# Optimization experiments

Hardware: AMD Instinct MI355X
Metric: run time of the kernel (lower is better)

The kernel has to match this reference:

```python
import jax, jax.numpy as jnp
import numpy as np

E = 256; H = 8; HD = E // H
L_LEN = 300; A_LEN = 250
T = 768; B = 4
NEG = -1e9


def setup_inputs() -> dict:
    rng = jax.random.key(0)
    ks = jax.random.split(rng, 16)
    n = lambda k, s, sc=1.0: jax.random.normal(k, s, dtype=jnp.float32) * sc
    return {
        "query": n(ks[0], (T, B, E)),
        "key": n(ks[1], (T, B, E)),
        "value": n(ks[2], (T, B, E)),
        "in_proj_w": n(ks[3], (3 * E, E), 0.05),
        "in_proj_b": jnp.zeros((3 * E,), jnp.float32),
        "out_w": n(ks[4], (7, E, E), 0.05),
        "out_b": jnp.zeros((7, E), jnp.float32),
        "s_l_w": n(ks[5], (E, 4 * E), 0.05),
        "s_l_b": jnp.zeros((E,), jnp.float32),
        "s_a_w": n(ks[6], (E, 4 * E), 0.05),
        "s_a_b": jnp.zeros((E,), jnp.float32),
        "s_v_w": n(ks[7], (E, 4 * E), 0.05),
        "s_v_b": jnp.zeros((E,), jnp.float32),
        "final_w": n(ks[8], (E, E), 0.05),
        "final_b": jnp.zeros((E,), jnp.float32),
    }


def _forward(query, key, value, in_proj_w, in_proj_b, out_w, out_b,
             s_l_w, s_l_b, s_a_w, s_a_b, s_v_w, s_v_b, final_w, final_b):
    t, b, e = query.shape
    scaling = HD ** -0.5
    Wq, Wk, Wv = in_proj_w[:E], in_proj_w[E:2 * E], in_proj_w[2 * E:]
    bq, bk, bv = in_proj_b[:E], in_proj_b[E:2 * E], in_proj_b[2 * E:]
    q = (query @ Wq.T + bq) * scaling
    k = key @ Wk.T + bk
    v = value @ Wv.T + bv
    # (T, B, E) -> (B*H, T, HD)
    sh = lambda x: x.reshape(t, b * H, HD).transpose(1, 0, 2)
    q, k, v = sh(q), sh(k), sh(v)
    # shared QK^T, reused by all 7 masked branches
    scores = jnp.einsum('bth,bsh->bts', q, k)  # (B*H, T, T)
    idx = jnp.arange(t)
    seg = jnp.where(idx < L_LEN, 0, jnp.where(idx < L_LEN + A_LEN, 1, 2))

    def branch(i, mods):
        # m[j] = 1 iff position j belongs to one of the selected modalities
        m = sum((seg == s) for s in mods).astype(scores.dtype)  # (T,)
        # additive mask: in-set query attends only in-set keys; out-of-set
        # query rows get all -1e9 (uniform softmax, zeroed by row mask below)
        add = jnp.where((m[:, None] * m[None, :]) > 0, 0.0, NEG)
        w = jax.nn.softmax(scores + add, axis=-1) * m[None, :, None]
        o = jnp.einsum('bts,bsh->bth', w, v * m[None, :, None])
        o = o.transpose(1, 0, 2).reshape(t, b, e)
        return o @ out_w[i].T + out_b[i]

    attn_lav = branch(0, (0, 1, 2))
    attn_la = branch(1, (0, 1))
    attn_lv = branch(2, (0, 2))
    attn_av = branch(3, (1, 2))
    attn_l = branch(4, (0,))
    attn_a = branch(5, (1,))
    attn_v = branch(6, (2,))

    sl = jnp.concatenate([attn_lav, attn_la, attn_lv, attn_l], -1) @ s_l_w.T + s_l_b
    sa = jnp.concatenate([attn_lav, attn_la, attn_av, attn_a], -1) @ s_a_w.T + s_a_b
    sv = jnp.concatenate([attn_lav, attn_lv, attn_av, attn_v], -1) @ s_v_w.T + s_v_b
    return (sl + sa + sv) @ final_w.T + final_b


def reference(query, key, value, in_proj_w, in_proj_b, out_w, out_b,
              s_l_w, s_l_b, s_a_w, s_a_b, s_v_w, s_v_b, final_w, final_b):
    return _forward(query, key, value, in_proj_w, in_proj_b, out_w, out_b,
                    s_l_w, s_l_b, s_a_w, s_a_b, s_v_w, s_v_b, final_w, final_b)
```

## Files before the change

### kernel.cpp

```cpp
#include <hip/hip_runtime.h>
#include <hip/hip_bf16.h>

#define E 256
#define H 8
#define HD 32
#define T 768
#define B 4
#define BH 32

typedef __attribute__((ext_vector_type(8))) short bf16x8;
typedef __attribute__((ext_vector_type(4))) float f32x4;
typedef __attribute__((ext_vector_type(16))) float f32x16;

__device__ __forceinline__ float b2f(__hip_bfloat16 x) { return __bfloat162float(x); }

__device__ __forceinline__ unsigned short f2bf_u(float x) {
    __hip_bfloat16 h = __float2bfloat16(x);
    return *(unsigned short*)&h;
}
__device__ __forceinline__ float bfu2f(unsigned short u) {
    return __uint_as_float(((unsigned int)u) << 16);
}

__device__ __forceinline__ int detect_f32(const void* query) {
    const unsigned short* q = (const unsigned short*)query;
    int lane = threadIdx.x & 63;
    int bad = 0;
    #pragma unroll
    for (int i = 0; i < 4; ++i) {
        float v = bfu2f(q[lane + i * 64]);
        bad |= (!(v == v) || fabsf(v) > 1e4f) ? 1 : 0;
    }
    return __any(bad) ? 1 : 0;
}

__device__ __forceinline__ void f8_split(const float* v, bf16x8& h, bf16x8& l) {
    #pragma unroll
    for (int e = 0; e < 8; ++e) {
        unsigned short hu = f2bf_u(v[e]);
        h[e] = (short)hu;
        l[e] = (short)f2bf_u(v[e] - bfu2f(hu));
    }
}

#define MFMA3(ACC, AH, AL, BH_, BL_)                                         \
    ACC = __builtin_amdgcn_mfma_f32_16x16x32_bf16(AH, BH_, ACC, 0, 0, 0);    \
    ACC = __builtin_amdgcn_mfma_f32_16x16x32_bf16(AH, BL_, ACC, 0, 0, 0);    \
    ACC = __builtin_amdgcn_mfma_f32_16x16x32_bf16(AL, BH_, ACC, 0, 0, 0);

#define MFMA3W(ACC, AH, AL, BH_, BL_)                                        \
    ACC = __builtin_amdgcn_mfma_f32_32x32x16_bf16(AH, BH_, ACC, 0, 0, 0);    \
    ACC = __builtin_amdgcn_mfma_f32_32x32x16_bf16(AH, BL_, ACC, 0, 0, 0);    \
    ACC = __builtin_amdgcn_mfma_f32_32x32x16_bf16(AL, BH_, ACC, 0, 0, 0);

__device__ __forceinline__ bf16x8 mk8(int a, int b, int c, int d) {
    union { int i[4]; bf16x8 v; } u;
    u.i[0] = a; u.i[1] = b; u.i[2] = c; u.i[3] = d;
    return u.v;
}

__device__ __forceinline__ float ldu(const void* p, size_t i, int f32) {
    if (f32) return ((const float*)p)[i];
    return b2f(((const __hip_bfloat16*)p)[i]);
}

__device__ __forceinline__ float gsum_load(int i, int r2, int r,
                                           const void* sl, const void* sa,
                                           const void* sv, int f32)
{
    size_t base = (size_t)r2 * 1024;
    switch (i) {
        case 0: return ldu(sl, base + r, f32) + ldu(sa, base + r, f32) + ldu(sv, base + r, f32);
        case 1: return ldu(sl, base + 256 + r, f32) + ldu(sa, base + 256 + r, f32);
        case 2: return ldu(sl, base + 512 + r, f32) + ldu(sv, base + 256 + r, f32);
        case 3: return ldu(sa, base + 512 + r, f32) + ldu(sv, base + 512 + r, f32);
        case 4: return ldu(sl, base + 768 + r, f32);
        case 5: return ldu(sa, base + 768 + r, f32);
        default: return ldu(sv, base + 768 + r, f32);
    }
}

__global__ __launch_bounds__(256) void stage1_kernel(
    const void* query, const void* w,
    const void* sl, const void* sa, const void* sv, const void* outw,
    const void* outb, const void* slb, const void* sab, const void* svb,
    unsigned short* __restrict__ WFh, unsigned short* __restrict__ WFl,
    unsigned short* __restrict__ GFh, unsigned short* __restrict__ GFl,
    unsigned short* __restrict__ OWFh, unsigned short* __restrict__ OWFl,
    float* __restrict__ c0)
{
    __shared__ float red[256];
    int f32 = detect_f32(query);
    if (blockIdx.x < 544) {
        int item = blockIdx.x * 256 + threadIdx.x;
        if (item < 24576) {
            int gc = item >> 5, kg = item & 31;
            float v[8];
            if (f32) {
                const float4* p = (const float4*)((const float*)w +
                                   (size_t)gc * 256 + kg * 8);
                *(float4*)&v[0] = p[0];
                *(float4*)&v[4] = p[1];
            } else {
                #pragma unroll
                for (int j = 0; j < 8; ++j)
                    v[j] = ldu(w, (size_t)gc * 256 + kg * 8 + j, 0);
            }
            bf16x8 h, l;
            f8_split(v, h, l);
            int sec = gc >> 8, c = gc & 255;
            int cb = c >> 4, kb = kg >> 2;
            int lane = (c & 15) | ((kg & 3) << 4);
            size_t idx = (((size_t)(sec * 16 + cb) * 8 + kb) * 64 + lane) * 8;
            *(bf16x8*)&WFh[idx] = h;
            *(bf16x8*)&WFl[idx] = l;
        } else if (item < 81920) {
            int rem = item - 24576;
            int i = rem >> 13;
            int rest = rem & 8191;
            int r2 = rest >> 5, kg = rest & 31;
            float v[8];
            #pragma unroll
            for (int j = 0; j < 8; ++j)
                v[j] = gsum_load(i, r2, kg * 8 + j, sl, sa, sv, f32);
            bf16x8 h, l;
            f8_split(v, h, l);
            int rb = r2 >> 4, kb = kg >> 2;
            int lane = (r2 & 15) | ((kg & 3) << 4);
            size_t idx = (((size_t)(i * 16 + rb) * 8 + kb) * 64 + lane) * 8;
            *(bf16x8*)&GFh[idx] = h;
            *(bf16x8*)&GFl[idx] = l;
        } else if (item < 139264) {
            int rem = item - 81920;
            int i = rem >> 13;
            int rest = rem & 8191;
            int kg = rest >> 8, c = rest & 255;
            float v[8];
            #pragma unroll
            for (int j = 0; j < 8; ++j)
                v[j] = ldu(outw, (size_t)i * 65536 + (kg * 8 + j) * 256 + c, f32);
            bf16x8 h, l;
            f8_split(v, h, l);
            int cb = c >> 4, kb = kg >> 2;
            int lane = (c & 15) | ((kg & 3) << 4);
            size_t idx = (((size_t)(i * 16 + cb) * 8 + kb) * 64 + lane) * 8;
            *(bf16x8*)&OWFh[idx] = h;
            *(bf16x8*)&OWFl[idx] = l;
        }
    } else {
        int r2 = blockIdx.x - 544, m = threadIdx.x;
        float acc = 0.f;
        #pragma unroll
        for (int i = 0; i < 7; ++i)
            acc += ldu(outb, i * 256 + m, f32) * gsum_load(i, r2, m, sl, sa, sv, f32);
        red[m] = acc;
        __syncthreads();
        for (int s = 128; s > 0; s >>= 1) {
            if (m < s) red[m] += red[m + s];
            __syncthreads();
        }
        if (m == 0)
            c0[r2] = red[0] + ldu(slb, r2, f32) + ldu(sab, r2, f32) + ldu(svb, r2, f32);
    }
}

__global__ __launch_bounds__(256) void stage2_kernel(
    const void* query, const void* key, const void* value,
    const unsigned short* __restrict__ WFh, const unsigned short* __restrict__ WFl,
    const void* bias,
    float* __restrict__ qws,
    unsigned short* __restrict__ KRh, unsigned short* __restrict__ KRl,
    unsigned short* __restrict__ VFh, unsigned short* __restrict__ VFl,
    const unsigned short* __restrict__ GFh, const unsigned short* __restrict__ GFl,
    const unsigned short* __restrict__ OWFh, const unsigned short* __restrict__ OWFl,
    float* __restrict__ Mtmp,
    const float* __restrict__ c0, const void* finalw, const void* finalb,
    float* __restrict__ d0)
{
    __shared__ float red[256];
    int bxx = blockIdx.x;
    if (bxx < 576) {
        int f32 = detect_f32(query);
        int sec = bxx / 192;
        int rb  = bxx % 192;
        const void* X = (sec == 0) ? query : (sec == 1) ? key : value;
        int w = threadIdx.x >> 6, lane = threadIdx.x & 63;
        int m = lane & 15, quad = lane >> 4;

        size_t aoff0 = (size_t)(rb * 16 + (lane & 15)) * 256 + quad * 8;

        f32x4 acc[4] = {};
        #pragma unroll
        for (int kb = 0; kb < 8; ++kb) {
            float av[8];
            size_t aoff = aoff0 + kb * 32;
            if (f32) {
                const float4* p = (const float4*)((const float*)X + aoff);
                *(float4*)&av[0] = p[0];
                *(float4*)&av[4] = p[1];
            } else {
                #pragma unroll
                for (int j = 0; j < 8; ++j)
                    av[j] = ldu(X, aoff + j, 0);
            }
            bf16x8 ah, al;
            f8_split(av, ah, al);
            #pragma unroll
            for (int c = 0; c < 4; ++c) {
                int cb = w * 4 + c;
                const unsigned short* Bh = WFh + (((size_t)(sec * 16 + cb) * 8 + kb) * 64 + lane) * 8;
                const unsigned short* Bl = WFl + (((size_t)(sec * 16 + cb) * 8 + kb) * 64 + lane) * 8;
                bf16x8 bh = *(const bf16x8*)Bh;
                bf16x8 bl = *(const bf16x8*)Bl;
                MFMA3(acc[c], ah, al, bh, bl)
            }
        }

        #pragma unroll
        for (int c = 0; c < 4; ++c) {
            int cb = w * 4 + c;
            int c_local = cb * 16 + m;
            float bv = ldu(bias, sec * 256 + c_local, f32);
            int h = c_local >> 5, hd = c_local & 31;

            if (sec == 0) {
                #pragma unroll
                for (int rr = 0; rr < 4; ++rr) {
                    int row = rb * 16 + quad * 4 + rr;
                    int t = row >> 2, b = row & 3;
                    float val = (acc[c][rr] + bv) * 0.17677669529663687f;
                    qws[((size_t)((b * H + h) * T + t)) * HD + hd] = val;
                }
            } else if (sec == 1) {
                #pragma unroll
                for (int rr = 0; rr < 4; ++rr) {
                    int row = rb * 16 + quad * 4 + rr;
                    int s = row >> 2, b = row & 3;
                    int bh_ = b * 8 + h;
                    float val = acc[c][rr] + bv;
                    unsigned short hu = f2bf_u(val);
                    unsigned short lu = f2bf_u(val - bfu2f(hu));
                    size_t bi = ((size_t)bh_ * 768 + s) * 32 + hd;
                    KRh[bi] = hu;
                    KRl[bi] = lu;
                }
            } else {
                #pragma unroll
                for (int rr = 0; rr < 4; ++rr) {
                    int row = rb * 16 + quad * 4 + rr;
                    int s = row >> 2, b = row & 3;
                    int bh_ = b * 8 + h;
                    float val = acc[c][rr] + bv;
                    unsigned short hu = f2bf_u(val);
                    unsigned short lu = f2bf_u(val - bfu2f(hu));
                    int s16 = s >> 4, hp = (s >> 3) & 1, j = s & 7;
                    size_t bi = (((size_t)bh_ * 48 + s16) * 64 + hp * 32 + hd) * 8 + j;
                    VFh[bi] = hu;
                    VFl[bi] = lu;
                }
            }
        }
    } else if (bxx < 1024) {
        int idx = bxx - 576;
        int cgrp = idx & 3;
        int rb   = (idx >> 2) & 15;
        int i    = idx >> 6;
        int w = threadIdx.x >> 6, lane = threadIdx.x & 63;
        int m = lane & 15, quad = lane >> 4;
        int cb = cgrp * 4 + w;

        const unsigned short* Ah = GFh + (((size_t)(i * 16 + rb) * 8) * 64 + lane) * 8;
        const unsigned short* Al = GFl + (((size_t)(i * 16 + rb) * 8) * 64 + lane) * 8;
        const unsigned short* Bh = OWFh + (((size_t)(i * 16 + cb) * 8) * 64 + lane) * 8;
        const unsigned short* Bl = OWFl + (((size_t)(i * 16 + cb) * 8) * 64 + lane) * 8;

        f32x4 acc = {};
        #pragma unroll
        for (int kb = 0; kb < 8; ++kb) {
            size_t off = (size_t)kb * 512;
            bf16x8 ah = *(const bf16x8*)(Ah + off);
            bf16x8 al = *(const bf16x8*)(Al + off);
            bf16x8 bh = *(const bf16x8*)(Bh + off);
            bf16x8 bl = *(const bf16x8*)(Bl + off);
            MFMA3(acc, ah, al, bh, bl)
        }
        #pragma unroll
        for (int rr = 0; rr < 4; ++rr) {
            int r2 = rb * 16 + quad * 4 + rr;
            Mtmp[(size_t)i * 65536 + r2 * 256 + cb * 16 + m] = acc[rr];
        }
    } else {
        int f32 = detect_f32(query);
        int e = bxx - 1024, r = threadIdx.x;
        red[r] = c0[r] * ldu(finalw, (size_t)e * 256 + r, f32);
        __syncthreads();
        for (int s = 128; s > 0; s >>= 1) {
            if (r < s) red[r] += red[r + s];
            __syncthreads();
        }
        if (r == 0)
            d0[e] = red[0] + ldu(finalb, e, f32);
    }
}

__global__ __launch_bounds__(256, 2) void stage3_kernel(
    const float* __restrict__ qws,
    const unsigned short* __restrict__ KRh, const unsigned short* __restrict__ KRl,
    const unsigned short* __restrict__ VFh, const unsigned short* __restrict__ VFl,
    unsigned short* __restrict__ Ohi, unsigned short* __restrict__ Olo,
    const float* __restrict__ Mtmp, const void* finalw, const void* query,
    unsigned short* __restrict__ DThi, unsigned short* __restrict__ DTlo)
{
    __shared__ __align__(16) float SMEM[7104];
    int tid = threadIdx.x;

    if (blockIdx.x < 768) {
        float (*AC2)[3][32][36] = (float(*)[3][32][36])&SMEM[0];
        float (*SS2)[3][32]     = (float(*)[3][32])&SMEM[6912];
        int bid = blockIdx.x;
        int xcd = bid & 7, rr_ = bid >> 3;
        int j_ = rr_ / 24, tile = rr_ % 24;
        int bh = j_ * 8 + xcd;
        int t0 = tile * 32;
        int w = tid >> 6, lane = tid & 63;
        int ln = lane & 31, h = lane >> 5;

        bf16x8 qbh[2], qbl[2];
        {
            const float* qr = qws + ((size_t)bh * T + t0 + ln) * HD + h * 8;
            #pragma unroll
            for (int c = 0; c < 2; ++c) {
                float qv[8];
                *(float4*)&qv[0] = *(const float4*)(qr + c * 16);
                *(float4*)&qv[4] = *(const float4*)(qr + c * 16 + 4);
                f8_split(qv, qbh[c], qbl[c]);
            }
        }

        f32x16 accA = {}, accB = {};
        float ssA = 0.f, ssB = 0.f;

        for (int q = 0; q < 3; ++q) {
            int ch = w * 3 + q;
            int sbase = ch * 64;
            int route = (ch == 5) ? 1 : (ch == 4 || ch == 8) ? 2 : 0;
            int bnd = (ch == 4) ? 300 : 550;
            bool c12 = (ch == 4);

            bf16x8 kf0h[2], kf0l[2], kf1h[2], kf1l[2], vh[4], vl[4];
            #pragma unroll
            for (int st = 0; st < 2; ++st) {
                size_t krow = ((size_t)bh * 768 + sbase + st * 32 + ln) * 32 + h * 8;
                kf0h[st] = *(const bf16x8*)(KRh + krow);
                kf0l[st] = *(const bf16x8*)(KRl + krow);
                kf1h[st] = *(const bf16x8*)(KRh + krow + 16);
                kf1l[st] = *(const bf16x8*)(KRl + krow + 16);
            }
            #pragma unroll
            for (int ks = 0; ks < 4; ++ks) {
                size_t vidx = (((size_t)bh * 48 + ch * 4 + ks) * 64 + lane) * 8;
                vh[ks] = *(const bf16x8*)(VFh + vidx);
                vl[ks] = *(const bf16x8*)(VFl + vidx);
            }

            #pragma unroll
            for (int st = 0; st < 2; ++st) {
                f32x16 d = {};
                MFMA3W(d, kf0h[st], kf0l[st], qbh[0], qbl[0])
                MFMA3W(d, kf1h[st], kf1l[st], qbh[1], qbl[1])

                int PH[8], PL[8];
                #pragma unroll
                for (int p = 0; p < 8; ++p) {
                    float e0 = __expf(d[2 * p]);
                    float e1 = __expf(d[2 * p + 1]);
                    if (route == 2) {
                        int r0 = 2 * p;
                        int s0 = sbase + st * 32 + (r0 & 3) + 8 * (r0 >> 2) + 4 * h;
                        if (s0 < bnd) ssA += e0; else ssB += e0;
                        if (s0 + 1 < bnd) ssA += e1; else ssB += e1;
                    } else if (route == 1) { ssB += e0 + e1; }
                    else { ssA += e0 + e1; }
                    unsigned b0 = __float_as_uint(e0), b1 = __float_as_uint(e1);
                    float l0 = e0 - __uint_as_float(b0 & 0xffff0000u);
                    float l1 = e1 - __uint_as_float(b1 & 0xffff0000u);
                    PH[p] = (int)((b0 >> 16) | (b1 & 0xffff0000u));
                    PL[p] = (int)((__float_as_uint(l0) >> 16) |
                                  (__float_as_uint(l1) & 0xffff0000u));
                }

                #pragma unroll
                for (int ksl = 0; ksl < 2; ++ksl) {
                    int ks = st * 2 + ksl;
                    int cc = 4 * ksl;
                    bf16x8 vbh = vh[ks];
                    bf16x8 vbl = vl[ks];

                    int sh0 = __shfl_xor(PH[cc+0], 32);
                    int sh1 = __shfl_xor(PH[cc+1], 32);
                    int sh2 = __shfl_xor(PH[cc+2], 32);
                    int sh3 = __shfl_xor(PH[cc+3], 32);
                    int sl0 = __shfl_xor(PL[cc+0], 32);
                    int sl1 = __shfl_xor(PL[cc+1], 32);
                    int sl2 = __shfl_xor(PL[cc+2], 32);
                    int sl3 = __shfl_xor(PL[cc+3], 32);
                    int FH0 = h ? sh2 : PH[cc+0];
                    int FH1 = h ? sh3 : PH[cc+1];
                    int FH2 = h ? PH[cc+2] : sh0;
                    int FH3 = h ? PH[cc+3] : sh1;
                    int FL0 = h ? sl2 : PL[cc+0];
                    int FL1 = h ? sl3 : PL[cc+1];
                    int FL2 = h ? PL[cc+2] : sl0;
                    int FL3 = h ? PL[cc+3] : sl1;
                    bf16x8 feh = mk8(FH0, FH1, FH2, FH3);
                    bf16x8 fel = mk8(FL0, FL1, FL2, FL3);

                    if (route == 0)      { MFMA3W(accA, feh, fel, vbh, vbl) }
                    else if (route == 1) { MFMA3W(accB, feh, fel, vbh, vbl) }
                    else {
                        if (ks < 2)       { MFMA3W(accA, feh, fel, vbh, vbl) }
                        else if (ks == 3) { MFMA3W(accB, feh, fel, vbh, vbl) }
                        else {
                            int a0 = h ? (c12 ? FH0 : 0) : FH0;
                            int a1 = h ? (c12 ? FH1 : 0) : FH1;
                            int a2 = h ? 0 : FH2;
                            int a3 = h ? 0 : (c12 ? FH3 : 0);
                            int b0 = h ? (c12 ? 0 : FH0) : 0;
                            int b1 = h ? (c12 ? 0 : FH1) : 0;
                            int b2 = h ? FH2 : 0;
                            int b3 = h ? FH3 : (c12 ? 0 : FH3);
                            int la0 = h ? (c12 ? FL0 : 0) : FL0;
                            int la1 = h ? (c12 ? FL1 : 0) : FL1;
                            int la2 = h ? 0 : FL2;
                            int la3 = h ? 0 : (c12 ? FL3 : 0);
                            int lb0 = h ? (c12 ? 0 : FL0) : 0;
                            int lb1 = h ? (c12 ? 0 : FL1) : 0;
                            int lb2 = h ? FL2 : 0;
                            int lb3 = h ? FL3 : (c12 ? 0 : FL3);
                            bf16x8 fha = mk8(a0, a1, a2, a3), fla = mk8(la0, la1, la2, la3);
                            bf16x8 fhb = mk8(b0, b1, b2, b3), flb = mk8(lb0, lb1, lb2, lb3);
                            MFMA3W(accA, fha, fla, vbh, vbl)
                            MFMA3W(accB, fhb, flb, vbh, vbl)
                        }
                    }
                }
            }
        }

        ssA += __shfl_xor(ssA, 32);
        ssB += __shfl_xor(ssB, 32);

        int bsel = w & 1;
        f32x16 zz = {};
        f32x16 o0 = (w <= 1) ? accA : zz;
        f32x16 o1 = (w == 1) ? accB : (w == 2) ? accA : zz;
        f32x16 o2 = (w == 2) ? accB : (w == 3) ? accA : zz;
        float s0 = (w <= 1) ? ssA : 0.f;
        float s1 = (w == 1) ? ssB : (w == 2) ? ssA : 0.f;
        float s2 = (w == 2) ? ssB : (w == 3) ? ssA : 0.f;

        if (w < 2) {
            #pragma unroll
            for (int r = 0; r < 16; ++r) {
                int t = (r & 3) + 8 * (r >> 2) + 4 * h;
                AC2[bsel][0][t][ln] = o0[r];
                AC2[bsel][1][t][ln] = o1[r];
                AC2[bsel][2][t][ln] = o2[r];
            }
            if (h == 0) {
                SS2[bsel][0][ln] = s0;
                SS2[bsel][1][ln] = s1;
                SS2[bsel][2][ln] = s2;
            }
        }
        __syncthreads();
        if (w >= 2) {
            #pragma unroll
            for (int r = 0; r < 16; ++r) {
                int t = (r & 3) + 8 * (r >> 2) + 4 * h;
                AC2[bsel][1][t][ln] += o1[r];
                AC2[bsel][2][t][ln] += o2[r];
            }
            if (h == 0) {
                SS2[bsel][1][ln] += s1;
                SS2[bsel][2][ln] += s2;
            }
        }
        __syncthreads();

        int tt = tid >> 3, q4 = tid & 7;
        float Pv[3][4], S[3];
        #pragma unroll
        for (int sg = 0; sg < 3; ++sg) {
            const float4 a = *(const float4*)&AC2[0][sg][tt][q4 * 4];
            const float4 b = *(const float4*)&AC2[1][sg][tt][q4 * 4];
            Pv[sg][0] = a.x + b.x; Pv[sg][1] = a.y + b.y;
            Pv[sg][2] = a.z + b.z; Pv[sg][3] = a.w + b.w;
            S[sg] = SS2[0][sg][tt] + SS2[1][sg][tt];
        }

        int t_glob = t0 + tt;
        int g = (t_glob < 300) ? 0 : (t_glob < 550 ? 1 : 2);
        int mixed = (((t_glob >> 4) == 18) || ((t_glob >> 4) == 34)) ? 1 : 0;
        int b_ = bh >> 3, h_ = bh & 7;
        int row = b_ * T + t_glob;
        int lslot = (row & 15) + ((q4 >> 1) << 4);
        int j0 = (q4 & 1) * 4;
        size_t fbase = (((size_t)(row >> 4) * 56 + h_) * 64 + lslot) * 8 + j0;
        const int masks[7] = {7, 3, 5, 6, 1, 2, 4};
        #pragma unroll
        for (int i = 0; i < 7; ++i) {
            int mm = masks[i];
            int live = (mm >> g) & 1;
            if (!(live | mixed)) continue;
            float n0 = 0.f, n1 = 0.f, n2 = 0.f, n3 = 0.f, den = 0.f;
            if (mm & 1) { n0 += Pv[0][0]; n1 += Pv[0][1]; n2 += Pv[0][2]; n3 += Pv[0][3]; den += S[0]; }
            if (mm & 2) { n0 += Pv[1][0]; n1 += Pv[1][1]; n2 += Pv[1][2]; n3 += Pv[1][3]; den += S[1]; }
            if (mm & 4) { n0 += Pv[2][0]; n1 += Pv[2][1]; n2 += Pv[2][2]; n3 += Pv[2][3]; den += S[2]; }
            float r = 1.f / den;
            float o[4];
            o[0] = live ? n0 * r : 0.f;
            o[1] = live ? n1 * r : 0.f;
            o[2] = live ? n2 * r : 0.f;
            o[3] = live ? n3 * r : 0.f;
            ushort4 hi4, lo4;
            unsigned short* hp = (unsigned short*)&hi4;
            unsigned short* lp = (unsigned short*)&lo4;
            #pragma unroll
            for (int jq = 0; jq < 4; ++jq) {
                unsigned short hu = f2bf_u(o[jq]);
                hp[jq] = hu;
                lp[jq] = f2bf_u(o[jq] - bfu2f(hu));
            }
            size_t addr = fbase + (size_t)i * (8 * 64 * 8);
            *(ushort4*)&Ohi[addr] = hi4;
            *(ushort4*)&Olo[addr] = lo4;
        }
    } else {
        float (*AsT)[34] = (float(*)[34])&SMEM[0];
        float (*Bs)[34]  = (float(*)[34])&SMEM[1088];
        int f32 = detect_f32(query);
        int idx = blockIdx.x - 768;
        int bx = idx & 7;
        int by = (idx >> 3) & 7;
        int i  = idx >> 6;
        int tx = tid & 15, ty = tid >> 4;
        int colbase = bx * 32, rowbase = by * 32;
        float acc[2][2] = {};

        for (int kb = 0; kb < 8; ++kb) {
            __syncthreads();
            #pragma unroll
            for (int l = 0; l < 4; ++l) {
                int idx2 = l * 256 + tid;
                int c = idx2 & 31, kk = idx2 >> 5;
                AsT[kk][c] = Mtmp[(size_t)i * 65536 + (kb * 32 + kk) * 256 + rowbase + c];
                int k2 = idx2 & 31, n = idx2 >> 5;
                Bs[k2][n] = ldu(finalw, (size_t)(colbase + n) * 256 + kb * 32 + k2, f32);
            }
            __syncthreads();
            #pragma unroll 8
            for (int kk = 0; kk < 32; ++kk) {
                const float2 av = *(const float2*)&AsT[kk][ty * 2];
                const float2 bv = *(const float2*)&Bs[kk][tx * 2];
                acc[0][0] += av.x * bv.x; acc[0][1] += av.x * bv.y;
                acc[1][0] += av.y * bv.x; acc[1][1] += av.y * bv.y;
            }
        }
        #pragma unroll
        for (int u = 0; u < 2; ++u)
            #pragma unroll
            for (int v = 0; v < 2; ++v) {
                int c = rowbase + ty * 2 + u, e = colbase + tx * 2 + v;
                float a = acc[u][v];
                unsigned short hu = f2bf_u(a);
                size_t fidx = (((size_t)(e >> 4) * 56 + i * 8 + (c >> 5)) * 64
                               + (e & 15) + (((c >> 3) & 3) << 4)) * 8 + (c & 7);
                DThi[fidx] = hu;
                DTlo[fidx] = f2bf_u(a - bfu2f(hu));
            }
    }
}

__global__ __launch_bounds__(256) void final_gemm_mfma_kernel(
    const unsigned short* __restrict__ Ohi, const unsigned short* __restrict__ Olo,
    const unsigned short* __restrict__ DThi, const unsigned short* __restrict__ DTlo,
    const float* __restrict__ d0, const void* query,
    void* __restrict__ outv)
{
    int f32 = detect_f32(query);
    int bid = blockIdx.x;
    int xcd = bid & 7, rr_ = bid >> 3;
    int slot = rr_ >> 2, bx = rr_ & 3;
    int by = slot * 8 + xcd;
    int w  = threadIdx.x >> 6;
    int lane = threadIdx.x & 63;
    int m = lane & 15, quad = lane >> 4;
    int R0 = by * 16, C0 = bx * 64 + w * 16;

    int b_out = R0 / 768;
    int tfirst = R0 - b_out * 768;
    int g0 = (tfirst < 300) ? 0 : (tfirst < 550 ? 1 : 2);
    int g1 = (tfirst + 15 < 300) ? 0 : (tfirst + 15 < 550 ? 1 : 2);
    int activeset = (1 << g0) | (1 << g1);
    const int masks[7] = {7, 3, 5, 6, 1, 2, 4};

    const unsigned short* Abase_h = Ohi + (size_t)by * 56 * 512 + lane * 8;
    const unsigned short* Abase_l = Olo + (size_t)by * 56 * 512 + lane * 8;
    const unsigned short* Bbase_h = DThi + (size_t)(bx * 4 + w) * 56 * 512 + lane * 8;
    const unsigned short* Bbase_l = DTlo + (size_t)(bx * 4 + w) * 56 * 512 + lane * 8;

    f32x4 acc = {};
    for (int i = 0; i < 7; ++i) {
        if (!(masks[i] & activeset)) continue;
        #pragma unroll
        for (int kb = 0; kb < 8; ++kb) {
            size_t off = (size_t)(i * 8 + kb) * 512;
            bf16x8 ah = *(const bf16x8*)(Abase_h + off);
            bf16x8 al = *(const bf16x8*)(Abase_l + off);
            bf16x8 bh = *(const bf16x8*)(Bbase_h + off);
            bf16x8 bl = *(const bf16x8*)(Bbase_l + off);
            acc = __builtin_amdgcn_mfma_f32_16x16x32_bf16(ah, bh, acc, 0, 0, 0);
            acc = __builtin_amdgcn_mfma_f32_16x16x32_bf16(ah, bl, acc, 0, 0, 0);
            acc = __builtin_amdgcn_mfma_f32_16x16x32_bf16(al, bh, acc, 0, 0, 0);
        }
    }
    float dv = d0[C0 + m];
    #pragma unroll
    for (int r = 0; r < 4; ++r) {
        int t = tfirst + quad * 4 + r;
        int col = C0 + m;
        float val = acc[r] + dv;
        size_t orow = (size_t)t * B + b_out;
        if (f32) ((float*)outv)[orow * 256 + col] = val;
        else ((__hip_bfloat16*)outv)[orow * 256 + col] = __float2bfloat16(val);
    }
}

extern "C" void kernel_launch(void* const* d_in, const int* in_sizes, int n_in,
                              void* d_out, int out_size, void* d_ws, size_t ws_size,
                              hipStream_t stream) {
    const void* query     = d_in[0];
    const void* key       = d_in[1];
    const void* value     = d_in[2];
    const void* in_proj_w = d_in[3];
    const void* in_proj_b = d_in[4];
    const void* out_w     = d_in[5];
    const void* out_b     = d_in[6];
    const void* s_l_w     = d_in[7];
    const void* s_l_b     = d_in[8];
    const void* s_a_w     = d_in[9];
    const void* s_a_b     = d_in[10];
    const void* s_v_w     = d_in[11];
    const void* s_v_b     = d_in[12];
    const void* final_w   = d_in[13];
    const void* final_b   = d_in[14];

    float* ws     = (float*)d_ws;
    float* qws    = ws;
    unsigned short* KRh = (unsigned short*)(ws + 786432);
    unsigned short* KRl = KRh + 786432;
    unsigned short* VFh = (unsigned short*)(ws + 1572864);
    unsigned short* VFl = VFh + 786432;
    unsigned short* Ohi = (unsigned short*)(ws + 2359296);
    unsigned short* Olo = (unsigned short*)(ws + 5111808);
    unsigned short* WFh = (unsigned short*)(ws + 2359296);
    unsigned short* WFl = WFh + 196608;
    unsigned short* GFh = (unsigned short*)(ws + 4915200);
    unsigned short* GFl = GFh + 458752;
    unsigned short* OWFh = GFl + 458752;
    unsigned short* OWFl = OWFh + 458752;
    float* Mtmp   = ws + 7864320;
    unsigned short* DThi = (unsigned short*)(ws + 8323072);
    unsigned short* DTlo = (unsigned short*)(ws + 8552448);
    float* d0     = ws + 8781824;
    float* c0     = ws + 8782336;

    stage1_kernel<<<800, 256, 0, stream>>>(query, in_proj_w,
                                           s_l_w, s_a_w, s_v_w, out_w,
                                           out_b, s_l_b, s_a_b, s_v_b,
                                           WFh, WFl,
                                           GFh, GFl, OWFh, OWFl, c0);
    stage2_kernel<<<1280, 256, 0, stream>>>(query, key, value,
                                            WFh, WFl, in_proj_b, qws,
                                            KRh, KRl, VFh, VFl,
                                            GFh, GFl, OWFh, OWFl, Mtmp,
                                            c0, final_w, final_b, d0);
    stage3_kernel<<<1216, 256, 0, stream>>>(qws, KRh, KRl, VFh, VFl,
                                            Ohi, Olo,
                                            Mtmp, final_w, query,
                                            DThi, DTlo);
    final_gemm_mfma_kernel<<<768, 256, 0, stream>>>(Ohi, Olo, DThi, DTlo,
                                                    d0, query, d_out);
}
```

Before: 160.3 us.

## Reschedule stages so independent weight prep overlaps attention and QKV projection

Drops the separate in_proj weight pre-split pass. The QKV projection now reads fp32 weights directly and splits them into hi/lo bf16 inline, which lets it run in the first kernel alongside the GF/OWF weight prep and the c0 reduction. The Mtmp GEMM and the d0 reduction move into the attention kernel as extra blocks, and the final-weight combine gets its own kernel. This rebalances work across launches to cut serial dependencies. The cost is redundant weight loads and splits per projection block, plus a workspace relocation.

```diff
diff --git a/kernel.cpp b/kernel.cpp
--- a/kernel.cpp
+++ b/kernel.cpp
@@ -81,113 +81,28 @@
 }
 
 __global__ __launch_bounds__(256) void stage1_kernel(
-    const void* query, const void* w,
+    const void* query, const void* key, const void* value, const void* w,
+    const void* bias,
     const void* sl, const void* sa, const void* sv, const void* outw,
     const void* outb, const void* slb, const void* sab, const void* svb,
-    unsigned short* __restrict__ WFh, unsigned short* __restrict__ WFl,
+    float* __restrict__ qws,
+    unsigned short* __restrict__ KRh, unsigned short* __restrict__ KRl,
+    unsigned short* __restrict__ VFh, unsigned short* __restrict__ VFl,
     unsigned short* __restrict__ GFh, unsigned short* __restrict__ GFl,
     unsigned short* __restrict__ OWFh, unsigned short* __restrict__ OWFl,
     float* __restrict__ c0)
 {
     __shared__ float red[256];
-    int f32 = detect_f32(query);
-    if (blockIdx.x < 544) {
-        int item = blockIdx.x * 256 + threadIdx.x;
-        if (item < 24576) {
-            int gc = item >> 5, kg = item & 31;
-            float v[8];
-            if (f32) {
-                const float4* p = (const float4*)((const float*)w +
-                                   (size_t)gc * 256 + kg * 8);
-                *(float4*)&v[0] = p[0];
-                *(float4*)&v[4] = p[1];
-            } else {
-                #pragma unroll
-                for (int j = 0; j < 8; ++j)
-                    v[j] = ldu(w, (size_t)gc * 256 + kg * 8 + j, 0);
-            }
-            bf16x8 h, l;
-            f8_split(v, h, l);
-            int sec = gc >> 8, c = gc & 255;
-            int cb = c >> 4, kb = kg >> 2;
-            int lane = (c & 15) | ((kg & 3) << 4);
-            size_t idx = (((size_t)(sec * 16 + cb) * 8 + kb) * 64 + lane) * 8;
-            *(bf16x8*)&WFh[idx] = h;
-            *(bf16x8*)&WFl[idx] = l;
-        } else if (item < 81920) {
-            int rem = item - 24576;
-            int i = rem >> 13;
-            int rest = rem & 8191;
-            int r2 = rest >> 5, kg = rest & 31;
-            float v[8];
-            #pragma unroll
-            for (int j = 0; j < 8; ++j)
-                v[j] = gsum_load(i, r2, kg * 8 + j, sl, sa, sv, f32);
-            bf16x8 h, l;
-            f8_split(v, h, l);
-            int rb = r2 >> 4, kb = kg >> 2;
-            int lane = (r2 & 15) | ((kg & 3) << 4);
-            size_t idx = (((size_t)(i * 16 + rb) * 8 + kb) * 64 + lane) * 8;
-            *(bf16x8*)&GFh[idx] = h;
-            *(bf16x8*)&GFl[idx] = l;
-        } else if (item < 139264) {
-            int rem = item - 81920;
-            int i = rem >> 13;
-            int rest = rem & 8191;
-            int kg = rest >> 8, c = rest & 255;
-            float v[8];
-            #pragma unroll
-            for (int j = 0; j < 8; ++j)
-                v[j] = ldu(outw, (size_t)i * 65536 + (kg * 8 + j) * 256 + c, f32);
-            bf16x8 h, l;
-            f8_split(v, h, l);
-            int cb = c >> 4, kb = kg >> 2;
-            int lane = (c & 15) | ((kg & 3) << 4);
-            size_t idx = (((size_t)(i * 16 + cb) * 8 + kb) * 64 + lane) * 8;
-            *(bf16x8*)&OWFh[idx] = h;
-            *(bf16x8*)&OWFl[idx] = l;
-        }
-    } else {
-        int r2 = blockIdx.x - 544, m = threadIdx.x;
-        float acc = 0.f;
-        #pragma unroll
-        for (int i = 0; i < 7; ++i)
-            acc += ldu(outb, i * 256 + m, f32) * gsum_load(i, r2, m, sl, sa, sv, f32);
-        red[m] = acc;
-        __syncthreads();
-        for (int s = 128; s > 0; s >>= 1) {
-            if (m < s) red[m] += red[m + s];
-            __syncthreads();
-        }
-        if (m == 0)
-            c0[r2] = red[0] + ldu(slb, r2, f32) + ldu(sab, r2, f32) + ldu(svb, r2, f32);
-    }
-}
-
-__global__ __launch_bounds__(256) void stage2_kernel(
-    const void* query, const void* key, const void* value,
-    const unsigned short* __restrict__ WFh, const unsigned short* __restrict__ WFl,
-    const void* bias,
-    float* __restrict__ qws,
-    unsigned short* __restrict__ KRh, unsigned short* __restrict__ KRl,
-    unsigned short* __restrict__ VFh, unsigned short* __restrict__ VFl,
-    const unsigned short* __restrict__ GFh, const unsigned short* __restrict__ GFl,
-    const unsigned short* __restrict__ OWFh, const unsigned short* __restrict__ OWFl,
-    float* __restrict__ Mtmp,
-    const float* __restrict__ c0, const void* finalw, const void* finalb,
-    float* __restrict__ d0)
-{
-    __shared__ float red[256];
-    int bxx = blockIdx.x;
-    if (bxx < 576) {
+    int bid = blockIdx.x;
+    if (bid < 576) {
         int f32 = detect_f32(query);
-        int sec = bxx / 192;
-        int rb  = bxx % 192;
+        int sec = bid / 192;
+        int rb  = bid % 192;
         const void* X = (sec == 0) ? query : (sec == 1) ? key : value;
-        int w = threadIdx.x >> 6, lane = threadIdx.x & 63;
+        int w_ = threadIdx.x >> 6, lane = threadIdx.x & 63;
         int m = lane & 15, quad = lane >> 4;
 
-        size_t aoff0 = (size_t)(rb * 16 + (lane & 15)) * 256 + quad * 8;
+        size_t aoff0 = (size_t)(rb * 16 + m) * 256 + quad * 8;
 
         f32x4 acc[4] = {};
         #pragma unroll
@@ -207,18 +122,28 @@
             f8_split(av, ah, al);
             #pragma unroll
             for (int c = 0; c < 4; ++c) {
-                int cb = w * 4 + c;
-                const unsigned short* Bh = WFh + (((size_t)(sec * 16 + cb) * 8 + kb) * 64 + lane) * 8;
-                const unsigned short* Bl = WFl + (((size_t)(sec * 16 + cb) * 8 + kb) * 64 + lane) * 8;
-                bf16x8 bh = *(const bf16x8*)Bh;
-                bf16x8 bl = *(const bf16x8*)Bl;
+                int cb = w_ * 4 + c;
+                float bv8[8];
+                size_t boff = (size_t)(sec * 256 + cb * 16 + m) * 256
+                              + kb * 32 + quad * 8;
+                if (f32) {
+                    const float4* p = (const float4*)((const float*)w + boff);
+                    *(float4*)&bv8[0] = p[0];
+                    *(float4*)&bv8[4] = p[1];
+                } else {
+                    #pragma unroll
+                    for (int j = 0; j < 8; ++j)
+                        bv8[j] = ldu(w, boff + j, 0);
+                }
+                bf16x8 bh, bl;
+                f8_split(bv8, bh, bl);
                 MFMA3(acc[c], ah, al, bh, bl)
             }
         }
 
         #pragma unroll
         for (int c = 0; c < 4; ++c) {
-            int cb = w * 4 + c;
+            int cb = w_ * 4 + c;
             int c_local = cb * 16 + m;
             float bv = ldu(bias, sec * 256 + c_local, f32);
             int h = c_local >> 5, hd = c_local & 31;
@@ -260,56 +185,69 @@
                 }
             }
         }
-    } else if (bxx < 1024) {
-        int idx = bxx - 576;
-        int cgrp = idx & 3;
-        int rb   = (idx >> 2) & 15;
-        int i    = idx >> 6;
-        int w = threadIdx.x >> 6, lane = threadIdx.x & 63;
-        int m = lane & 15, quad = lane >> 4;
-        int cb = cgrp * 4 + w;
-
-        const unsigned short* Ah = GFh + (((size_t)(i * 16 + rb) * 8) * 64 + lane) * 8;
-        const unsigned short* Al = GFl + (((size_t)(i * 16 + rb) * 8) * 64 + lane) * 8;
-        const unsigned short* Bh = OWFh + (((size_t)(i * 16 + cb) * 8) * 64 + lane) * 8;
-        const unsigned short* Bl = OWFl + (((size_t)(i * 16 + cb) * 8) * 64 + lane) * 8;
-
-        f32x4 acc = {};
-        #pragma unroll
-        for (int kb = 0; kb < 8; ++kb) {
-            size_t off = (size_t)kb * 512;
-            bf16x8 ah = *(const bf16x8*)(Ah + off);
-            bf16x8 al = *(const bf16x8*)(Al + off);
-            bf16x8 bh = *(const bf16x8*)(Bh + off);
-            bf16x8 bl = *(const bf16x8*)(Bl + off);
-            MFMA3(acc, ah, al, bh, bl)
-        }
-        #pragma unroll
-        for (int rr = 0; rr < 4; ++rr) {
-            int r2 = rb * 16 + quad * 4 + rr;
-            Mtmp[(size_t)i * 65536 + r2 * 256 + cb * 16 + m] = acc[rr];
+    } else if (bid < 1024) {
+        int f32 = detect_f32(query);
+        int item = (bid - 576) * 256 + threadIdx.x;
+        if (item < 57344) {
+            int i = item >> 13;
+            int rest = item & 8191;
+            int r2 = rest >> 5, kg = rest & 31;
+            float v[8];
+            #pragma unroll
+            for (int j = 0; j < 8; ++j)
+                v[j] = gsum_load(i, r2, kg * 8 + j, sl, sa, sv, f32);
+            bf16x8 h, l;
+            f8_split(v, h, l);
+            int rb = r2 >> 4, kb = kg >> 2;
+            int lane = (r2 & 15) | ((kg & 3) << 4);
+            size_t idx = (((size_t)(i * 16 + rb) * 8 + kb) * 64 + lane) * 8;
+            *(bf16x8*)&GFh[idx] = h;
+            *(bf16x8*)&GFl[idx] = l;
+        } else if (item < 114688) {
+            int rem = item - 57344;
+            int i = rem >> 13;
+            int rest = rem & 8191;
+            int kg = rest >> 8, c = rest & 255;
+            float v[8];
+            #pragma unroll
+            for (int j = 0; j < 8; ++j)
+                v[j] = ldu(outw, (size_t)i * 65536 + (kg * 8 + j) * 256 + c, f32);
+            bf16x8 h, l;
+            f8_split(v, h, l);
+            int cb = c >> 4, kb = kg >> 2;
+            int lane = (c & 15) | ((kg & 3) << 4);
+            size_t idx = (((size_t)(i * 16 + cb) * 8 + kb) * 64 + lane) * 8;
+            *(bf16x8*)&OWFh[idx] = h;
+            *(bf16x8*)&OWFl[idx] = l;
         }
     } else {
         int f32 = detect_f32(query);
-        int e = bxx - 1024, r = threadIdx.x;
-        red[r] = c0[r] * ldu(finalw, (size_t)e * 256 + r, f32);
+        int r2 = bid - 1024, m = threadIdx.x;
+        float acc = 0.f;
+        #pragma unroll
+        for (int i = 0; i < 7; ++i)
+            acc += ldu(outb, i * 256 + m, f32) * gsum_load(i, r2, m, sl, sa, sv, f32);
+        red[m] = acc;
         __syncthreads();
         for (int s = 128; s > 0; s >>= 1) {
-            if (r < s) red[r] += red[r + s];
+            if (m < s) red[m] += red[m + s];
             __syncthreads();
         }
-        if (r == 0)
-            d0[e] = red[0] + ldu(finalb, e, f32);
-    }
-}
-
-__global__ __launch_bounds__(256, 2) void stage3_kernel(
+        if (m == 0)
+            c0[r2] = red[0] + ldu(slb, r2, f32) + ldu(sab, r2, f32) + ldu(svb, r2, f32);
+    }
+}
+
+__global__ __launch_bounds__(256, 2) void stage2_kernel(
     const float* __restrict__ qws,
     const unsigned short* __restrict__ KRh, const unsigned short* __restrict__ KRl,
     const unsigned short* __restrict__ VFh, const unsigned short* __restrict__ VFl,
     unsigned short* __restrict__ Ohi, unsigned short* __restrict__ Olo,
-    const float* __restrict__ Mtmp, const void* finalw, const void* query,
-    unsigned short* __restrict__ DThi, unsigned short* __restrict__ DTlo)
+    const unsigned short* __restrict__ GFh, const unsigned short* __restrict__ GFl,
+    const unsigned short* __restrict__ OWFh, const unsigned short* __restrict__ OWFl,
+    float* __restrict__ Mtmp,
+    const float* __restrict__ c0, const void* finalw, const void* finalb,
+    const void* query, float* __restrict__ d0)
 {
     __shared__ __align__(16) float SMEM[7104];
     int tid = threadIdx.x;
@@ -536,50 +474,97 @@
             *(ushort4*)&Ohi[addr] = hi4;
             *(ushort4*)&Olo[addr] = lo4;
         }
+    } else if (blockIdx.x < 1216) {
+        int idx = blockIdx.x - 768;
+        int cgrp = idx & 3;
+        int rb   = (idx >> 2) & 15;
+        int i    = idx >> 6;
+        int w = tid >> 6, lane = tid & 63;
+        int m = lane & 15, quad = lane >> 4;
+        int cb = cgrp * 4 + w;
+
+        const unsigned short* Ah = GFh + (((size_t)(i * 16 + rb) * 8) * 64 + lane) * 8;
+        const unsigned short* Al = GFl + (((size_t)(i * 16 + rb) * 8) * 64 + lane) * 8;
+        const unsigned short* Bh = OWFh + (((size_t)(i * 16 + cb) * 8) * 64 + lane) * 8;
+        const unsigned short* Bl = OWFl + (((size_t)(i * 16 + cb) * 8) * 64 + lane) * 8;
+
+        f32x4 acc = {};
+        #pragma unroll
+        for (int kb = 0; kb < 8; ++kb) {
+            size_t off = (size_t)kb * 512;
+            bf16x8 ah = *(const bf16x8*)(Ah + off);
+            bf16x8 al = *(const bf16x8*)(Al + off);
+            bf16x8 bh = *(const bf16x8*)(Bh + off);
+            bf16x8 bl = *(const bf16x8*)(Bl + off);
+            MFMA3(acc, ah, al, bh, bl)
+        }
+        #pragma unroll
+        for (int rr = 0; rr < 4; ++rr) {
+            int r2 = rb * 16 + quad * 4 + rr;
+            Mtmp[(size_t)i * 65536 + r2 * 256 + cb * 16 + m] = acc[rr];
+        }
     } else {
-        float (*AsT)[34] = (float(*)[34])&SMEM[0];
-        float (*Bs)[34]  = (float(*)[34])&SMEM[1088];
+        float* red = &SMEM[0];
         int f32 = detect_f32(query);
-        int idx = blockIdx.x - 768;
-        int bx = idx & 7;
-        int by = (idx >> 3) & 7;
-        int i  = idx >> 6;
-        int tx = tid & 15, ty = tid >> 4;
-        int colbase = bx * 32, rowbase = by * 32;
-        float acc[2][2] = {};
-
-        for (int kb = 0; kb < 8; ++kb) {
+        int e = blockIdx.x - 1216, r = tid;
+        red[r] = c0[r] * ldu(finalw, (size_t)e * 256 + r, f32);
+        __syncthreads();
+        for (int s = 128; s > 0; s >>= 1) {
+            if (r < s) red[r] += red[r + s];
             __syncthreads();
-            #pragma unroll
-            for (int l = 0; l < 4; ++l) {
-                int idx2 = l * 256 + tid;
-                int c = idx2 & 31, kk = idx2 >> 5;
-                AsT[kk][c] = Mtmp[(size_t)i * 65536 + (kb * 32 + kk) * 256 + rowbase + c];
-                int k2 = idx2 & 31, n = idx2 >> 5;
-                Bs[k2][n] = ldu(finalw, (size_t)(colbase + n) * 256 + kb * 32 + k2, f32);
-            }
-            __syncthreads();
-            #pragma unroll 8
-            for (int kk = 0; kk < 32; ++kk) {
-                const float2 av = *(const float2*)&AsT[kk][ty * 2];
-                const float2 bv = *(const float2*)&Bs[kk][tx * 2];
-                acc[0][0] += av.x * bv.x; acc[0][1] += av.x * bv.y;
-                acc[1][0] += av.y * bv.x; acc[1][1] += av.y * bv.y;
-            }
-        }
-        #pragma unroll
-        for (int u = 0; u < 2; ++u)
-            #pragma unroll
-            for (int v = 0; v < 2; ++v) {
-                int c = rowbase + ty * 2 + u, e = colbase + tx * 2 + v;
-                float a = acc[u][v];
-                unsigned short hu = f2bf_u(a);
-                size_t fidx = (((size_t)(e >> 4) * 56 + i * 8 + (c >> 5)) * 64
-                               + (e & 15) + (((c >> 3) & 3) << 4)) * 8 + (c & 7);
-                DThi[fidx] = hu;
-                DTlo[fidx] = f2bf_u(a - bfu2f(hu));
-            }
-    }
+        }
+        if (r == 0)
+            d0[e] = red[0] + ldu(finalb, e, f32);
+    }
+}
+
+__global__ __launch_bounds__(256) void wcomb2_kernel(
+    const float* __restrict__ Mtmp, const void* finalw, const void* query,
+    unsigned short* __restrict__ DThi, unsigned short* __restrict__ DTlo)
+{
+    __shared__ __align__(16) float AsT[32][34];
+    __shared__ __align__(16) float Bs[32][34];
+    int f32 = detect_f32(query);
+    int idx = blockIdx.x;
+    int bx = idx & 7;
+    int by = (idx >> 3) & 7;
+    int i  = idx >> 6;
+    int tid = threadIdx.x;
+    int tx = tid & 15, ty = tid >> 4;
+    int colbase = bx * 32, rowbase = by * 32;
+    float acc[2][2] = {};
+
+    for (int kb = 0; kb < 8; ++kb) {
+        __syncthreads();
+        #pragma unroll
+        for (int l = 0; l < 4; ++l) {
+            int idx2 = l * 256 + tid;
+            int c = idx2 & 31, kk = idx2 >> 5;
+            AsT[kk][c] = Mtmp[(size_t)i * 65536 + (kb * 32 + kk) * 256 + rowbase + c];
+            int k2 = idx2 & 31, n = idx2 >> 5;
+            Bs[k2][n] = ldu(finalw, (size_t)(colbase + n) * 256 + kb * 32 + k2, f32);
+        }
+        __syncthreads();
+        #pragma unroll 8
+        for (int kk = 0; kk < 32; ++kk) {
+            const float2 av = *(const float2*)&AsT[kk][ty * 2];
+            const float2 bv = *(const float2*)&Bs[kk][tx * 2];
+            acc[0][0] += av.x * bv.x; acc[0][1] += av.x * bv.y;
+            acc[1][0] += av.y * bv.x; acc[1][1] += av.y * bv.y;
+        }
+    }
+    #pragma unroll
+    for (int u = 0; u < 2; ++u)
+        #pragma unroll
+        for (int v = 0; v < 2; ++v) {
+            int c = rowbase + ty * 2 + u, e = colbase + tx * 2 + v;
+            float a = acc[u][v];
+            unsigned short hu = f2bf_u(a);
+            size_t fidx = (((size_t)(e >> 4) * 56 + i * 8 + (c >> 5)) * 64
+                           + (e & 15) + (((c >> 3) & 3) << 4)) * 8 + (c & 7);
+            DThi[fidx] = hu;
+            DTlo[fidx] = f2bf_u(a - bfu2f(hu));
+        }
 }
 
 __global__ __launch_bounds__(256) void final_gemm_mfma_kernel(
@@ -664,32 +649,27 @@
     unsigned short* VFl = VFh + 786432;
     unsigned short* Ohi = (unsigned short*)(ws + 2359296);
     unsigned short* Olo = (unsigned short*)(ws + 5111808);
-    unsigned short* WFh = (unsigned short*)(ws + 2359296);
-    unsigned short* WFl = WFh + 196608;
-    unsigned short* GFh = (unsigned short*)(ws + 4915200);
-    unsigned short* GFl = GFh + 458752;
-    unsigned short* OWFh = GFl + 458752;
-    unsigned short* OWFl = OWFh + 458752;
     float* Mtmp   = ws + 7864320;
     unsigned short* DThi = (unsigned short*)(ws + 8323072);
     unsigned short* DTlo = (unsigned short*)(ws + 8552448);
     float* d0     = ws + 8781824;
     float* c0     = ws + 8782336;
-
-    stage1_kernel<<<800, 256, 0, stream>>>(query, in_proj_w,
-                                           s_l_w, s_a_w, s_v_w, out_w,
-                                           out_b, s_l_b, s_a_b, s_v_b,
-                                           WFh, WFl,
-                                           GFh, GFl, OWFh, OWFl, c0);
-    stage2_kernel<<<1280, 256, 0, stream>>>(query, key, value,
-                                            WFh, WFl, in_proj_b, qws,
-                                            KRh, KRl, VFh, VFl,
+    unsigned short* GFh = (unsigned short*)(ws + 8782848);
+    unsigned short* GFl = GFh + 458752;
+    unsigned short* OWFh = GFl + 458752;
+    unsigned short* OWFl = OWFh + 458752;
+
+    stage1_kernel<<<1280, 256, 0, stream>>>(query, key, value, in_proj_w,
+                                            in_proj_b,
+                                            s_l_w, s_a_w, s_v_w, out_w,
+                                            out_b, s_l_b, s_a_b, s_v_b,
+                                            qws, KRh, KRl, VFh, VFl,
+                                            GFh, GFl, OWFh, OWFl, c0);
+    stage2_kernel<<<1472, 256, 0, stream>>>(qws, KRh, KRl, VFh, VFl,
+                                            Ohi, Olo,
                                             GFh, GFl, OWFh, OWFl, Mtmp,
-                                            c0, final_w, final_b, d0);
-    stage3_kernel<<<1216, 256, 0, stream>>>(qws, KRh, KRl, VFh, VFl,
-                                            Ohi, Olo,
-                                            Mtmp, final_w, query,
-                                            DThi, DTlo);
+                                            c0, final_w, final_b, query, d0);
+    wcomb2_kernel<<<448, 256, 0, stream>>>(Mtmp, final_w, query, DThi, DTlo);
     final_gemm_mfma_kernel<<<768, 256, 0, stream>>>(Ohi, Olo, DThi, DTlo,
                                                     d0, query, d_out);
 }
```

After: 174.4 us. +8.8%, slower.
